# Kernel optimization log

Hardware: AMD Instinct MI355X
Metric: run time of the kernel (lower is better)

## Reference

```python
import jax, jax.numpy as jnp
import numpy as np

V = 50000
D = 128
EF = 16
E = 800000
LN_EPS = 1e-5


def setup_inputs() -> dict:
    key = jax.random.key(0)
    ks = jax.random.split(key, 9)
    h = jax.random.normal(ks[0], (V, D), dtype=jnp.float32)
    edge_index = jax.random.randint(ks[1], (2, E), 0, V, dtype=jnp.int64)
    edge_attr = jax.random.normal(ks[2], (E, EF), dtype=jnp.float32)
    # msg_mlp = Linear(D+EF, D) -> ReLU -> Dropout(0) -> Linear(D, D)
    s1 = 1.0 / np.sqrt(D + EF)
    s2 = 1.0 / np.sqrt(D)
    W1 = jax.random.uniform(ks[3], (D + EF, D), minval=-s1, maxval=s1, dtype=jnp.float32)
    b1 = jax.random.uniform(ks[4], (D,), minval=-s1, maxval=s1, dtype=jnp.float32)
    W2 = jax.random.uniform(ks[5], (D, D), minval=-s2, maxval=s2, dtype=jnp.float32)
    b2 = jax.random.uniform(ks[6], (D,), minval=-s2, maxval=s2, dtype=jnp.float32)
    gamma = jnp.ones((D,), dtype=jnp.float32)
    beta = jnp.zeros((D,), dtype=jnp.float32)
    return {"h": h, "edge_index": edge_index, "edge_attr": edge_attr,
            "W1": W1, "b1": b1, "W2": W2, "b2": b2,
            "gamma": gamma, "beta": beta}


def _layer_norm(x, gamma, beta):
    mu = jnp.mean(x, axis=-1, keepdims=True)
    var = jnp.mean(jnp.square(x - mu), axis=-1, keepdims=True)
    return (x - mu) * jax.lax.rsqrt(var + LN_EPS) * gamma + beta


def reference(h, edge_index, edge_attr, W1, b1, W2, b2, gamma, beta):
    src, dst = edge_index[0], edge_index[1]
    # gather source node features, concat edge features: [E, D+EF]
    x = jnp.concatenate([h[src], edge_attr], axis=-1)
    # per-edge message MLP (dropout p=0 -> identity)
    msg = jax.nn.relu(x @ W1 + b1) @ W2 + b2  # [E, D]
    # scatter-add messages to destinations
    agg = jax.ops.segment_sum(msg, dst, num_segments=V)  # [V, D]
    # count initialized to ones BEFORE scatter_add -> denominator = 1 + in_degree
    deg = jax.ops.segment_sum(jnp.ones((E,), dtype=h.dtype), dst, num_segments=V)
    count = (1.0 + deg)[:, None]  # [V, 1]
    return _layer_norm(h + agg / count, gamma, beta)
```

## Files before the change

kernel.cpp:

```cpp
#include <hip/hip_runtime.h>
#include <hip/hip_bf16.h>

#define V 50000
#define D 128
#define EF 16
#define E_EDGES 800000
#define NT 12500
#define USTR 136
#define XESTR 40
#define CSTR 132
#define NSCAN 196
#define EGRID 1024
#define UGRID 782

typedef __attribute__((ext_vector_type(8))) __bf16 bf16x8;
typedef __attribute__((ext_vector_type(4))) float f32x4;

__device__ inline unsigned short f2bf(float f) {
    unsigned u = __float_as_uint(f);
    u += 0x7FFF + ((u >> 16) & 1);
    return (unsigned short)(u >> 16);
}
__device__ inline unsigned pack2(float a, float b) {
    return (unsigned)f2bf(a) | ((unsigned)f2bf(b) << 16);
}
__device__ inline float bf2f(unsigned short u) {
    return __uint_as_float((unsigned)u << 16);
}

__global__ __launch_bounds__(256)
void setup_kernel(const int* __restrict__ ei, int* __restrict__ cnt,
                  float* __restrict__ agg,
                  const float* __restrict__ W1, const float* __restrict__ W2,
                  unsigned short* __restrict__ W1p, unsigned short* __restrict__ W2p) {
    int idx = blockIdx.x * 256 + threadIdx.x;
    *(float4*)(agg + ((size_t)idx << 2)) = (float4){0.f, 0.f, 0.f, 0.f};
    if (idx < E_EDGES) atomicAdd(&cnt[ei[E_EDGES + idx]], 1);
    if (idx < 5 * 128 * 32) {
        int kb = idx >> 12, rem = idx & 4095;
        int n = rem >> 5, kk = rem & 31;
        int k = kb * 32 + kk;
        W1p[idx] = f2bf((k < D + EF) ? W1[k * D + n] : 0.0f);
    }
    if (idx < 4 * 128 * 32) {
        int kb = idx >> 12, rem = idx & 4095;
        int n = rem >> 5, kk = rem & 31;
        W2p[idx] = f2bf(W2[(kb * 32 + kk) * D + n]);
    }
}

__global__ __launch_bounds__(256)
void u_gemm_kernel(const float* __restrict__ h,
                   const unsigned short* __restrict__ W1p,
                   unsigned short* __restrict__ U) {
    __shared__ __align__(16) unsigned short Hs[64 * USTR];
    const int tid  = threadIdx.x;
    const int lane = tid & 63;
    const int wave = tid >> 6;
    const int nlo  = lane & 15;
    const int kq   = lane >> 4;
    const int er   = tid >> 4;
    const int ec   = tid & 15;
    const int gbase = blockIdx.x << 6;

    bf16x8 B1[4][2];
    #pragma unroll
    for (int t = 0; t < 2; ++t) {
        int n = wave * 32 + t * 16 + nlo;
        #pragma unroll
        for (int kb = 0; kb < 4; ++kb)
            B1[kb][t] = *(const bf16x8*)(W1p + ((kb << 7) + n) * 32 + (kq << 3));
    }

    #pragma unroll
    for (int m = 0; m < 4; ++m) {
        int row = er + m * 16;
        int grow = gbase + row;
        unsigned* o = (unsigned*)(Hs + row * USTR + (ec << 3));
        if (grow < V) {
            const float4* p = (const float4*)(h + (size_t)grow * D + (ec << 3));
            float4 v0 = p[0], v1 = p[1];
            o[0] = pack2(v0.x, v0.y); o[1] = pack2(v0.z, v0.w);
            o[2] = pack2(v1.x, v1.y); o[3] = pack2(v1.z, v1.w);
        } else {
            o[0] = 0u; o[1] = 0u; o[2] = 0u; o[3] = 0u;
        }
    }
    __syncthreads();

    f32x4 acc[4][2];
    #pragma unroll
    for (int mt = 0; mt < 4; ++mt)
        #pragma unroll
        for (int t = 0; t < 2; ++t)
            acc[mt][t] = (f32x4){0.f, 0.f, 0.f, 0.f};

    #pragma unroll
    for (int kb = 0; kb < 4; ++kb) {
        bf16x8 A[4];
        int ko = kb * 32 + (kq << 3);
        #pragma unroll
        for (int mt = 0; mt < 4; ++mt)
            A[mt] = *(const bf16x8*)(Hs + (mt * 16 + nlo) * USTR + ko);
        #pragma unroll
        for (int mt = 0; mt < 4; ++mt)
            #pragma unroll
            for (int t = 0; t < 2; ++t)
                acc[mt][t] = __builtin_amdgcn_mfma_f32_16x16x32_bf16(A[mt], B1[kb][t], acc[mt][t], 0, 0, 0);
    }

    #pragma unroll
    for (int mt = 0; mt < 4; ++mt)
        #pragma unroll
        for (int t = 0; t < 2; ++t)
            #pragma unroll
            for (int r = 0; r < 4; ++r) {
                int row = mt * 16 + (kq << 2) + r;
                int grow = gbase + row;
                int col = wave * 32 + t * 16 + nlo;
                if (grow < V)
                    U[(size_t)grow * D + col] = f2bf(acc[mt][t][r]);
            }
}

__device__ inline int block_excl_scan(int x, int t, int* ws) {
    int lane = t & 63, w = t >> 6;
    int inc = x;
    #pragma unroll
    for (int off = 1; off < 64; off <<= 1) {
        int y = __shfl_up(inc, off);
        if (lane >= off) inc += y;
    }
    if (lane == 63) ws[w] = inc;
    __syncthreads();
    if (t == 0) {
        int r = 0;
        #pragma unroll
        for (int i = 0; i < 4; ++i) { int c = ws[i]; ws[i] = r; r += c; }
    }
    __syncthreads();
    return inc - x + ws[w];
}

__global__ __launch_bounds__(256)
void scan1_kernel(const int* __restrict__ cnt, int* __restrict__ cursor,
                  int* __restrict__ bsum) {
    __shared__ int ws[4];
    __shared__ int tot;
    int t = threadIdx.x;
    int i = blockIdx.x * 256 + t;
    int x = (i < V) ? cnt[i] : 0;
    int ex = block_excl_scan(x, t, ws);
    if (i < V) cursor[i] = ex;
    if (t == 255) tot = ex + x;
    __syncthreads();
    if (t == 0) bsum[blockIdx.x] = tot;
}

__global__ __launch_bounds__(256)
void scatter_kernel(const int* __restrict__ ei, int* __restrict__ cursor,
                    const int* __restrict__ bsum,
                    int* __restrict__ srcs, int* __restrict__ dsts,
                    int* __restrict__ eidx) {
    __shared__ int ws[4];
    __shared__ int sboff[NSCAN];
    int t = threadIdx.x;
    int x = (t < NSCAN) ? bsum[t] : 0;
    int ex = block_excl_scan(x, t, ws);
    if (t < NSCAN) sboff[t] = ex;
    __syncthreads();
    int e = blockIdx.x * 256 + t;
    int d = ei[E_EDGES + e];
    int pos = atomicAdd(&cursor[d], 1) + sboff[d >> 8];
    srcs[pos] = ei[e];
    dsts[pos] = d;
    eidx[pos] = e;
}

__global__ __launch_bounds__(256, 4)
void edge_kernel(const unsigned short* __restrict__ U,
                 const float* __restrict__ ea,
                 const int* __restrict__ srcs, const int* __restrict__ dsts,
                 const int* __restrict__ eidx,
                 const unsigned short* __restrict__ W1p, const unsigned short* __restrict__ W2p,
                 const float* __restrict__ b1, const float* __restrict__ b2,
                 float* __restrict__ agg) {
    union SharedU {
        unsigned short Us[64 * USTR];
        float C[64 * CSTR];
    };
    __shared__ __align__(16) SharedU u;
    __shared__ __align__(16) unsigned short Xe[64 * XESTR];
    __shared__ int sDst[64];

    const int tid  = threadIdx.x;
    const int lane = tid & 63;
    const int wave = tid >> 6;
    const int nlo  = lane & 15;
    const int kq   = lane >> 4;
    const int er   = tid >> 4;
    const int ec   = tid & 15;
    const int ee   = tid >> 2;
    const int eq   = tid & 3;

    bf16x8 B1e[2], B2[4][2];
    float b1v[2], b2v[2];
    #pragma unroll
    for (int t = 0; t < 2; ++t) {
        int n = wave * 32 + t * 16 + nlo;
        b1v[t] = b1[n];
        b2v[t] = b2[n];
        B1e[t] = *(const bf16x8*)(W1p + ((4 << 7) + n) * 32 + (kq << 3));
        #pragma unroll
        for (int kb = 0; kb < 4; ++kb)
            B2[kb][t] = *(const bf16x8*)(W2p + ((kb << 7) + n) * 32 + (kq << 3));
    }

    {
        unsigned* xz = (unsigned*)Xe;
        int i0 = tid, i1 = tid + 256;
        xz[(i0 >> 3) * (XESTR / 2) + 8 + (i0 & 7)] = 0u;
        xz[(i1 >> 3) * (XESTR / 2) + 8 + (i1 & 7)] = 0u;
    }

    const int base0 = blockIdx.x << 6;
    int a0 = srcs[base0 + er];
    int a1 = srcs[base0 + er + 16];
    int a2 = srcs[base0 + er + 32];
    int a3 = srcs[base0 + er + 48];
    int aev = eidx[base0 + ee];
    int ddcur = dsts[base0 + lane];
    bf16x8 pf0 = *(const bf16x8*)(U + (size_t)a0 * D + (ec << 3));
    bf16x8 pf1 = *(const bf16x8*)(U + (size_t)a1 * D + (ec << 3));
    bf16x8 pf2 = *(const bf16x8*)(U + (size_t)a2 * D + (ec << 3));
    bf16x8 pf3 = *(const bf16x8*)(U + (size_t)a3 * D + (ec << 3));
    float4 pfe = *(const float4*)(ea + (size_t)aev * EF + (eq << 2));

    int n1 = blockIdx.x + EGRID;
    int nb1 = (n1 < NT ? n1 : blockIdx.x) << 6;
    int i1s0 = srcs[nb1 + er];
    int i1s1 = srcs[nb1 + er + 16];
    int i1s2 = srcs[nb1 + er + 32];
    int i1s3 = srcs[nb1 + er + 48];
    int i1e  = eidx[nb1 + ee];
    int i1d  = dsts[nb1 + lane];

    for (int tile = blockIdx.x; tile < NT; tile += EGRID) {
        int n2 = tile + 2 * EGRID;
        int nb2 = (n2 < NT ? n2 : tile) << 6;
        int i2s0 = srcs[nb2 + er];
        int i2s1 = srcs[nb2 + er + 16];
        int i2s2 = srcs[nb2 + er + 32];
        int i2s3 = srcs[nb2 + er + 48];
        int i2e  = eidx[nb2 + ee];
        int i2d  = dsts[nb2 + lane];

        if (tid < 64) sDst[tid] = ddcur;
        *(bf16x8*)(u.Us + er * USTR + (ec << 3))        = pf0;
        *(bf16x8*)(u.Us + (er + 16) * USTR + (ec << 3)) = pf1;
        *(bf16x8*)(u.Us + (er + 32) * USTR + (ec << 3)) = pf2;
        *(bf16x8*)(u.Us + (er + 48) * USTR + (ec << 3)) = pf3;
        {
            unsigned* xp = (unsigned*)Xe + ee * (XESTR / 2) + (eq << 1);
            xp[0] = pack2(pfe.x, pfe.y);
            xp[1] = pack2(pfe.z, pfe.w);
        }
        __syncthreads();

        bf16x8 q0 = *(const bf16x8*)(U + (size_t)i1s0 * D + (ec << 3));
        bf16x8 q1 = *(const bf16x8*)(U + (size_t)i1s1 * D + (ec << 3));
        bf16x8 q2 = *(const bf16x8*)(U + (size_t)i1s2 * D + (ec << 3));
        bf16x8 q3 = *(const bf16x8*)(U + (size_t)i1s3 * D + (ec << 3));
        float4 qe = *(const float4*)(ea + (size_t)i1e * EF + (eq << 2));
        int nextdd = i1d;

        f32x4 accE[4][2];
        #pragma unroll
        for (int mt = 0; mt < 4; ++mt)
            #pragma unroll
            for (int t = 0; t < 2; ++t)
                accE[mt][t] = (f32x4){0.f, 0.f, 0.f, 0.f};
        {
            bf16x8 A[4];
            #pragma unroll
            for (int mt = 0; mt < 4; ++mt)
                A[mt] = *(const bf16x8*)(Xe + (mt * 16 + nlo) * XESTR + (kq << 3));
            #pragma unroll
            for (int mt = 0; mt < 4; ++mt)
                #pragma unroll
                for (int t = 0; t < 2; ++t)
                    accE[mt][t] = __builtin_amdgcn_mfma_f32_16x16x32_bf16(A[mt], B1e[t], accE[mt][t], 0, 0, 0);
        }

        #pragma unroll
        for (int mt = 0; mt < 4; ++mt)
            #pragma unroll
            for (int t = 0; t < 2; ++t)
                #pragma unroll
                for (int r = 0; r < 4; ++r) {
                    int row = mt * 16 + (kq << 2) + r;
                    int col = wave * 32 + t * 16 + nlo;
                    unsigned short* yp = u.Us + row * USTR + col;
                    float y = fmaxf(bf2f(*yp) + accE[mt][t][r] + b1v[t], 0.0f);
                    *yp = f2bf(y);
                }
        __syncthreads();

        f32x4 acc2[4][2];
        #pragma unroll
        for (int mt = 0; mt < 4; ++mt)
            #pragma unroll
            for (int t = 0; t < 2; ++t)
                acc2[mt][t] = (f32x4){0.f, 0.f, 0.f, 0.f};

        #pragma unroll
        for (int kb = 0; kb < 4; ++kb) {
            bf16x8 A[4];
            int ko = kb * 32 + (kq << 3);
            #pragma unroll
            for (int mt = 0; mt < 4; ++mt)
                A[mt] = *(const bf16x8*)(u.Us + (mt * 16 + nlo) * USTR + ko);
            #pragma unroll
            for (int mt = 0; mt < 4; ++mt)
                #pragma unroll
                for (int t = 0; t < 2; ++t)
                    acc2[mt][t] = __builtin_amdgcn_mfma_f32_16x16x32_bf16(A[mt], B2[kb][t], acc2[mt][t], 0, 0, 0);
        }
        __syncthreads();

        #pragma unroll
        for (int mt = 0; mt < 4; ++mt)
            #pragma unroll
            for (int t = 0; t < 2; ++t)
                #pragma unroll
                for (int r = 0; r < 4; ++r) {
                    int row = mt * 16 + (kq << 2) + r;
                    int col = wave * 32 + t * 16 + nlo;
                    u.C[row * CSTR + col] = acc2[mt][t][r] + b2v[t];
                }
        __syncthreads();

        {
            int col = tid & 127;
            int rbase = (tid >> 7) << 5;
            float sum = 0.f;
            int cur = sDst[rbase];
            for (int i = 0; i < 32; ++i) {
                int row = rbase + i;
                int d = sDst[row];
                if (d != cur) {
                    atomicAdd(&agg[(size_t)cur * D + col], sum);
                    sum = 0.f;
                    cur = d;
                }
                sum += u.C[row * CSTR + col];
            }
            atomicAdd(&agg[(size_t)cur * D + col], sum);
        }
        __syncthreads();

        pf0 = q0; pf1 = q1; pf2 = q2; pf3 = q3; pfe = qe; ddcur = nextdd;
        i1s0 = i2s0; i1s1 = i2s1; i1s2 = i2s2; i1s3 = i2s3; i1e = i2e; i1d = i2d;
    }
}

__global__ __launch_bounds__(256)
void finalize_kernel(const float* __restrict__ h, const float* __restrict__ agg,
                     const int* __restrict__ cnt,
                     const float* __restrict__ gamma, const float* __restrict__ beta,
                     float* __restrict__ out) {
    int wave = threadIdx.x >> 6, lane = threadIdx.x & 63;
    int v = blockIdx.x * 4 + wave;
    if (v >= V) return;
    float inv = 1.0f / (1.0f + (float)cnt[v]);
    const float* hr = h + (size_t)v * D;
    const float* ar = agg + (size_t)v * D;
    float x0 = hr[lane]      + ar[lane]      * inv;
    float x1 = hr[lane + 64] + ar[lane + 64] * inv;
    float s = x0 + x1;
    #pragma unroll
    for (int m = 32; m; m >>= 1) s += __shfl_xor(s, m);
    float mu = s * (1.0f / 128.0f);
    float d0 = x0 - mu, d1 = x1 - mu;
    float vs = d0 * d0 + d1 * d1;
    #pragma unroll
    for (int m = 32; m; m >>= 1) vs += __shfl_xor(vs, m);
    float rs = rsqrtf(vs * (1.0f / 128.0f) + 1e-5f);
    out[(size_t)v * D + lane]      = d0 * rs * gamma[lane]      + beta[lane];
    out[(size_t)v * D + 64 + lane] = d1 * rs * gamma[lane + 64] + beta[lane + 64];
}

extern "C" void kernel_launch(void* const* d_in, const int* in_sizes, int n_in,
                              void* d_out, int out_size, void* d_ws, size_t ws_size,
                              hipStream_t stream) {
    const float* h     = (const float*)d_in[0];
    const int*   ei    = (const int*)d_in[1];
    const float* ea    = (const float*)d_in[2];
    const float* W1    = (const float*)d_in[3];
    const float* b1    = (const float*)d_in[4];
    const float* W2    = (const float*)d_in[5];
    const float* b2    = (const float*)d_in[6];
    const float* gamma = (const float*)d_in[7];
    const float* beta  = (const float*)d_in[8];
    float* out = (float*)d_out;

    char* ws = (char*)d_ws;
    float*          agg    = (float*)ws;
    int*            cnt    = (int*)(ws + 25600000);
    int*            cursor = (int*)(ws + 25800000);
    int*            bsum   = (int*)(ws + 26000000);
    int*            srcs   = (int*)(ws + 26000800);
    int*            dsts   = (int*)(ws + 29200800);
    int*            eidx   = (int*)(ws + 32400800);
    unsigned short* W1p    = (unsigned short*)(ws + 35600800);
    unsigned short* W2p    = (unsigned short*)(ws + 35641760);
    unsigned short* U      = (unsigned short*)(ws + 35674528);

    hipMemsetAsync(cnt, 0, 200000, stream);
    setup_kernel<<<6250, 256, 0, stream>>>(ei, cnt, agg, W1, W2, W1p, W2p);
    u_gemm_kernel<<<UGRID, 256, 0, stream>>>(h, W1p, U);
    scan1_kernel<<<NSCAN, 256, 0, stream>>>(cnt, cursor, bsum);
    scatter_kernel<<<3125, 256, 0, stream>>>(ei, cursor, bsum, srcs, dsts, eidx);
    edge_kernel<<<EGRID, 256, 0, stream>>>(U, ea, srcs, dsts, eidx, W1p, W2p, b1, b2, agg);
    finalize_kernel<<<12500, 256, 0, stream>>>(h, agg, cnt, gamma, beta, out);
}
```

Before: 319.8 us.

## Split LDS buffers, store messages as fp16, drop two barriers per tile

```diff
diff --git a/kernel.cpp b/kernel.cpp
--- a/kernel.cpp
+++ b/kernel.cpp
@@ -8,7 +8,7 @@
 #define NT 12500
 #define USTR 136
 #define XESTR 40
-#define CSTR 132
+#define CSTR 136
 #define NSCAN 196
 #define EGRID 1024
 #define UGRID 782
@@ -185,13 +185,10 @@
                  const unsigned short* __restrict__ W1p, const unsigned short* __restrict__ W2p,
                  const float* __restrict__ b1, const float* __restrict__ b2,
                  float* __restrict__ agg) {
-    union SharedU {
-        unsigned short Us[64 * USTR];
-        float C[64 * CSTR];
-    };
-    __shared__ __align__(16) SharedU u;
+    __shared__ __align__(16) unsigned short Us[64 * USTR];
+    __shared__ __align__(16) _Float16 Cs[64 * CSTR];
     __shared__ __align__(16) unsigned short Xe[64 * XESTR];
-    __shared__ int sDst[64];
+    __shared__ int sDst[2][64];
 
     const int tid  = threadIdx.x;
     const int lane = tid & 63;
@@ -245,6 +242,7 @@
     int i1e  = eidx[nb1 + ee];
     int i1d  = dsts[nb1 + lane];
 
+    int buf = 0;
     for (int tile = blockIdx.x; tile < NT; tile += EGRID) {
         int n2 = tile + 2 * EGRID;
         int nb2 = (n2 < NT ? n2 : tile) << 6;
@@ -255,11 +253,11 @@
         int i2e  = eidx[nb2 + ee];
         int i2d  = dsts[nb2 + lane];
 
-        if (tid < 64) sDst[tid] = ddcur;
-        *(bf16x8*)(u.Us + er * USTR + (ec << 3))        = pf0;
-        *(bf16x8*)(u.Us + (er + 16) * USTR + (ec << 3)) = pf1;
-        *(bf16x8*)(u.Us + (er + 32) * USTR + (ec << 3)) = pf2;
-        *(bf16x8*)(u.Us + (er + 48) * USTR + (ec << 3)) = pf3;
+        if (tid < 64) sDst[buf][tid] = ddcur;
+        *(bf16x8*)(Us + er * USTR + (ec << 3))        = pf0;
+        *(bf16x8*)(Us + (er + 16) * USTR + (ec << 3)) = pf1;
+        *(bf16x8*)(Us + (er + 32) * USTR + (ec << 3)) = pf2;
+        *(bf16x8*)(Us + (er + 48) * USTR + (ec << 3)) = pf3;
         {
             unsigned* xp = (unsigned*)Xe + ee * (XESTR / 2) + (eq << 1);
             xp[0] = pack2(pfe.x, pfe.y);
@@ -279,7 +277,9 @@
         for (int mt = 0; mt < 4; ++mt)
             #pragma unroll
             for (int t = 0; t < 2; ++t)
-                accE[mt][t] = (f32x4){0.f, 0.f, 0.f, 0.f};
+                #pragma unroll
+                for (int r = 0; r < 4; ++r)
+                    accE[mt][t][r] = bf2f(Us[(mt * 16 + (kq << 2) + r) * USTR + wave * 32 + t * 16 + nlo]);
         {
             bf16x8 A[4];
             #pragma unroll
@@ -300,9 +300,7 @@
                 for (int r = 0; r < 4; ++r) {
                     int row = mt * 16 + (kq << 2) + r;
                     int col = wave * 32 + t * 16 + nlo;
-                    unsigned short* yp = u.Us + row * USTR + col;
-                    float y = fmaxf(bf2f(*yp) + accE[mt][t][r] + b1v[t], 0.0f);
-                    *yp = f2bf(y);
+                    Us[row * USTR + col] = f2bf(fmaxf(accE[mt][t][r] + b1v[t], 0.0f));
                 }
         __syncthreads();
 
@@ -319,14 +317,13 @@
             int ko = kb * 32 + (kq << 3);
             #pragma unroll
             for (int mt = 0; mt < 4; ++mt)
-                A[mt] = *(const bf16x8*)(u.Us + (mt * 16 + nlo) * USTR + ko);
+                A[mt] = *(const bf16x8*)(Us + (mt * 16 + nlo) * USTR + ko);
             #pragma unroll
             for (int mt = 0; mt < 4; ++mt)
                 #pragma unroll
                 for (int t = 0; t < 2; ++t)
                     acc2[mt][t] = __builtin_amdgcn_mfma_f32_16x16x32_bf16(A[mt], B2[kb][t], acc2[mt][t], 0, 0, 0);
         }
-        __syncthreads();
 
         #pragma unroll
         for (int mt = 0; mt < 4; ++mt)
@@ -336,7 +333,7 @@
                 for (int r = 0; r < 4; ++r) {
                     int row = mt * 16 + (kq << 2) + r;
                     int col = wave * 32 + t * 16 + nlo;
-                    u.C[row * CSTR + col] = acc2[mt][t][r] + b2v[t];
+                    Cs[row * CSTR + col] = (_Float16)(acc2[mt][t][r] + b2v[t]);
                 }
         __syncthreads();
 
@@ -344,23 +341,22 @@
             int col = tid & 127;
             int rbase = (tid >> 7) << 5;
             float sum = 0.f;
-            int cur = sDst[rbase];
+            int cur = sDst[buf][rbase];
             for (int i = 0; i < 32; ++i) {
-                int row = rbase + i;
-                int d = sDst[row];
+                int d = sDst[buf][rbase + i];
                 if (d != cur) {
                     atomicAdd(&agg[(size_t)cur * D + col], sum);
                     sum = 0.f;
                     cur = d;
                 }
-                sum += u.C[row * CSTR + col];
+                sum += (float)Cs[(rbase + i) * CSTR + col];
             }
             atomicAdd(&agg[(size_t)cur * D + col], sum);
         }
-        __syncthreads();
 
         pf0 = q0; pf1 = q1; pf2 = q2; pf3 = q3; pfe = qe; ddcur = nextdd;
         i1s0 = i2s0; i1s1 = i2s1; i1s2 = i2s2; i1s3 = i2s3; i1e = i2e; i1d = i2d;
+        buf ^= 1;
     }
 }
 
```

Result: slower. 331.3 us (+3.6%).
